# Optimization experiments

Hardware: AMD Instinct MI355X
Metric: run time of the kernel (lower is better)

## Reference

```python
import jax, jax.numpy as jnp
import numpy as np


def setup_inputs() -> dict:
    key = jax.random.key(0)
    k1, k2 = jax.random.split(key)
    image_features = jax.random.normal(k1, (8192, 128), dtype=jnp.float32)
    gts = jax.random.normal(k2, (16384, 128), dtype=jnp.float32)
    return {"image_features": image_features, "gts": gts}


def reference(image_features, gts):
    # (same math as subtract-square-sum-sqrt, O(N*M) memory instead of O(N*M*D))
    x_sq = jnp.sum(image_features * image_features, axis=-1, keepdims=True)  # [N,1]
    g_sq = jnp.sum(gts * gts, axis=-1)[None, :]                              # [1,M]
    xg = jnp.einsum('nd,md->nm', image_features, gts)                        # [N,M]
    d2 = jnp.maximum(x_sq + g_sq - 2.0 * xg, 0.0)
    logits = -jnp.sqrt(d2)
    return logits
```

## Files before the change

kernel.cpp:

```cpp
#include <hip/hip_runtime.h>


#define N_IMG 8192
#define N_GTS 16384
#define K_DIM 128
#define BM 128
#define BN 128
#define LDS_K 64
#define LDAH 72

typedef __attribute__((ext_vector_type(8))) short short8;
typedef __attribute__((ext_vector_type(4))) float f32x4;

__device__ __forceinline__ unsigned short f2bf(float x) {
    unsigned int u = __float_as_uint(x);
    u += 0x7FFFu + ((u >> 16) & 1u);
    return (unsigned short)(u >> 16);
}

__global__ __launch_bounds__(256, 2)
void l2sim_kernel(const float* __restrict__ A, const float* __restrict__ G,
                  float* __restrict__ out)
{
    __shared__ short a_s[BM][LDAH];
    __shared__ short b_s[BN][LDAH];
    __shared__ float xsq_s[2][BM];
    __shared__ float gsq_s[2][BN];

    const int t  = threadIdx.x;
    const int bm = blockIdx.y;
    const int bn = blockIdx.x;

    const int wave = t >> 6;
    const int lane = t & 63;
    const int wm   = (wave & 1) << 6;
    const int wn   = (wave >> 1) << 6;
    const int lm   = lane & 15;
    const int quad = lane >> 4;

    f32x4 acc[4][4] = {};

    #pragma unroll
    for (int h = 0; h < 2; ++h) {
        if (h) __syncthreads();

        {
            const float* gA = A + (size_t)bm * BM * K_DIM + h * LDS_K;
            #pragma unroll
            for (int i = 0; i < 8; ++i) {
                int f   = i * 256 + t;
                int row = f >> 4;
                int c4  = f & 15;
                float4 v = *(const float4*)(gA + (size_t)row * K_DIM + c4 * 4);
                float s = v.x*v.x + v.y*v.y + v.z*v.z + v.w*v.w;
                s += __shfl_down(s, 8, 16);
                s += __shfl_down(s, 4, 16);
                s += __shfl_down(s, 2, 16);
                s += __shfl_down(s, 1, 16);
                short4 bv;
                bv.x = (short)f2bf(v.x);
                bv.y = (short)f2bf(v.y);
                bv.z = (short)f2bf(v.z);
                bv.w = (short)f2bf(v.w);
                *(short4*)&a_s[row][c4 * 4] = bv;
                if ((t & 15) == 0) xsq_s[h][row] = s;
            }
        }
        {
            const float* gB = G + (size_t)bn * BN * K_DIM + h * LDS_K;
            #pragma unroll
            for (int i = 0; i < 8; ++i) {
                int f   = i * 256 + t;
                int row = f >> 4;
                int c4  = f & 15;
                float4 v = *(const float4*)(gB + (size_t)row * K_DIM + c4 * 4);
                float s = v.x*v.x + v.y*v.y + v.z*v.z + v.w*v.w;
                s += __shfl_down(s, 8, 16);
                s += __shfl_down(s, 4, 16);
                s += __shfl_down(s, 2, 16);
                s += __shfl_down(s, 1, 16);
                short4 bv;
                bv.x = (short)f2bf(v.x);
                bv.y = (short)f2bf(v.y);
                bv.z = (short)f2bf(v.z);
                bv.w = (short)f2bf(v.w);
                *(short4*)&b_s[row][c4 * 4] = bv;
                if ((t & 15) == 0) gsq_s[h][row] = s;
            }
        }
        __syncthreads();

        #pragma unroll
        for (int ks = 0; ks < 2; ++ks) {
            short8 af[4], bfr[4];
            #pragma unroll
            for (int mi = 0; mi < 4; ++mi)
                af[mi] = *(const short8*)&a_s[wm + mi * 16 + lm][ks * 32 + quad * 8];
            #pragma unroll
            for (int ni = 0; ni < 4; ++ni)
                bfr[ni] = *(const short8*)&b_s[wn + ni * 16 + lm][ks * 32 + quad * 8];
            #pragma unroll
            for (int mi = 0; mi < 4; ++mi)
                #pragma unroll
                for (int ni = 0; ni < 4; ++ni)
                    acc[mi][ni] = __builtin_amdgcn_mfma_f32_16x16x32_bf16(
                        af[mi], bfr[ni], acc[mi][ni], 0, 0, 0);
        }
    }

    float* outBase = out + (size_t)bm * BM * N_GTS + (size_t)bn * BN;
    #pragma unroll
    for (int mi = 0; mi < 4; ++mi) {
        #pragma unroll
        for (int r = 0; r < 4; ++r) {
            int m_loc = wm + mi * 16 + quad * 4 + r;
            float xs = xsq_s[0][m_loc] + xsq_s[1][m_loc];
            float* orow = outBase + (size_t)m_loc * N_GTS;
            #pragma unroll
            for (int ni = 0; ni < 4; ++ni) {
                int n_loc = wn + ni * 16 + lm;
                float gs = gsq_s[0][n_loc] + gsq_s[1][n_loc];
                float d2 = fmaxf(xs + gs - 2.0f * acc[mi][ni][r], 0.0f);
                orow[n_loc] = -sqrtf(d2);
            }
        }
    }
}

extern "C" void kernel_launch(void* const* d_in, const int* in_sizes, int n_in,
                              void* d_out, int out_size, void* d_ws, size_t ws_size,
                              hipStream_t stream) {
    const float* A = (const float*)d_in[0];
    const float* G = (const float*)d_in[1];
    float* out = (float*)d_out;
    dim3 grid(N_GTS / BN, N_IMG / BM);
    l2sim_kernel<<<grid, 256, 0, stream>>>(A, G, out);
}
```

Baseline: 796.9 us.

## Load MFMA fragments directly from global memory, dropping LDS staging and barriers

Each wave now reads its A and G fragments straight from global memory in MFMA layout, converts them with packed bf16 conversion instructions, and computes row norms in registers with cross-lane shuffles. This removes shared-memory staging, the block barriers and the software rounding routine. Occupancy hint rises to 3 blocks per CU. The cost is redundant global/L2 reads, since waves sharing a tile row or column reload the same data.

```diff
diff --git a/kernel.cpp b/kernel.cpp
--- a/kernel.cpp
+++ b/kernel.cpp
@@ -4,124 +4,90 @@
 #define N_IMG 8192
 #define N_GTS 16384
 #define K_DIM 128
-#define BM 128
-#define BN 128
-#define LDS_K 64
-#define LDAH 72
 
 typedef __attribute__((ext_vector_type(8))) short short8;
 typedef __attribute__((ext_vector_type(4))) float f32x4;
 
-__device__ __forceinline__ unsigned short f2bf(float x) {
-    unsigned int u = __float_as_uint(x);
-    u += 0x7FFFu + ((u >> 16) & 1u);
-    return (unsigned short)(u >> 16);
+__device__ __forceinline__ short8 cvt8(const float4& a, const float4& b) {
+    union { short8 s; unsigned int u[4]; } r;
+    asm("v_cvt_pk_bf16_f32 %0, %1, %2" : "=v"(r.u[0]) : "v"(a.x), "v"(a.y));
+    asm("v_cvt_pk_bf16_f32 %0, %1, %2" : "=v"(r.u[1]) : "v"(a.z), "v"(a.w));
+    asm("v_cvt_pk_bf16_f32 %0, %1, %2" : "=v"(r.u[2]) : "v"(b.x), "v"(b.y));
+    asm("v_cvt_pk_bf16_f32 %0, %1, %2" : "=v"(r.u[3]) : "v"(b.z), "v"(b.w));
+    return r.s;
 }
 
-__global__ __launch_bounds__(256, 2)
+__global__ __launch_bounds__(256, 3)
 void l2sim_kernel(const float* __restrict__ A, const float* __restrict__ G,
                   float* __restrict__ out)
 {
-    __shared__ short a_s[BM][LDAH];
-    __shared__ short b_s[BN][LDAH];
-    __shared__ float xsq_s[2][BM];
-    __shared__ float gsq_s[2][BN];
-
-    const int t  = threadIdx.x;
-    const int bm = blockIdx.y;
-    const int bn = blockIdx.x;
-
+    const int t    = threadIdx.x;
     const int wave = t >> 6;
     const int lane = t & 63;
-    const int wm   = (wave & 1) << 6;
-    const int wn   = (wave >> 1) << 6;
     const int lm   = lane & 15;
     const int quad = lane >> 4;
 
+    const int wtm = blockIdx.y * 128 + (wave & 1) * 64;
+    const int wtn = blockIdx.x * 128 + (wave >> 1) * 64;
+
+    const float* aRow[4];
+    const float* gRow[4];
+    #pragma unroll
+    for (int i = 0; i < 4; ++i) {
+        aRow[i] = A + (size_t)(wtm + i * 16 + lm) * K_DIM + quad * 8;
+        gRow[i] = G + (size_t)(wtn + i * 16 + lm) * K_DIM + quad * 8;
+    }
+
     f32x4 acc[4][4] = {};
+    float xsq[4] = {0.f, 0.f, 0.f, 0.f};
+    float gsq[4] = {0.f, 0.f, 0.f, 0.f};
 
     #pragma unroll
-    for (int h = 0; h < 2; ++h) {
-        if (h) __syncthreads();
-
-        {
-            const float* gA = A + (size_t)bm * BM * K_DIM + h * LDS_K;
-            #pragma unroll
-            for (int i = 0; i < 8; ++i) {
-                int f   = i * 256 + t;
-                int row = f >> 4;
-                int c4  = f & 15;
-                float4 v = *(const float4*)(gA + (size_t)row * K_DIM + c4 * 4);
-                float s = v.x*v.x + v.y*v.y + v.z*v.z + v.w*v.w;
-                s += __shfl_down(s, 8, 16);
-                s += __shfl_down(s, 4, 16);
-                s += __shfl_down(s, 2, 16);
-                s += __shfl_down(s, 1, 16);
-                short4 bv;
-                bv.x = (short)f2bf(v.x);
-                bv.y = (short)f2bf(v.y);
-                bv.z = (short)f2bf(v.z);
-                bv.w = (short)f2bf(v.w);
-                *(short4*)&a_s[row][c4 * 4] = bv;
-                if ((t & 15) == 0) xsq_s[h][row] = s;
-            }
+    for (int ks = 0; ks < 4; ++ks) {
+        short8 af[4], bfr[4];
+        #pragma unroll
+        for (int mi = 0; mi < 4; ++mi) {
+            float4 v0 = *(const float4*)(aRow[mi] + ks * 32);
+            float4 v1 = *(const float4*)(aRow[mi] + ks * 32 + 4);
+            xsq[mi] += v0.x*v0.x + v0.y*v0.y + v0.z*v0.z + v0.w*v0.w
+                     + v1.x*v1.x + v1.y*v1.y + v1.z*v1.z + v1.w*v1.w;
+            af[mi] = cvt8(v0, v1);
         }
-        {
-            const float* gB = G + (size_t)bn * BN * K_DIM + h * LDS_K;
-            #pragma unroll
-            for (int i = 0; i < 8; ++i) {
-                int f   = i * 256 + t;
-                int row = f >> 4;
-                int c4  = f & 15;
-                float4 v = *(const float4*)(gB + (size_t)row * K_DIM + c4 * 4);
-                float s = v.x*v.x + v.y*v.y + v.z*v.z + v.w*v.w;
-                s += __shfl_down(s, 8, 16);
-                s += __shfl_down(s, 4, 16);
-                s += __shfl_down(s, 2, 16);
-                s += __shfl_down(s, 1, 16);
-                short4 bv;
-                bv.x = (short)f2bf(v.x);
-                bv.y = (short)f2bf(v.y);
-                bv.z = (short)f2bf(v.z);
-                bv.w = (short)f2bf(v.w);
-                *(short4*)&b_s[row][c4 * 4] = bv;
-                if ((t & 15) == 0) gsq_s[h][row] = s;
-            }
+        #pragma unroll
+        for (int ni = 0; ni < 4; ++ni) {
+            float4 v0 = *(const float4*)(gRow[ni] + ks * 32);
+            float4 v1 = *(const float4*)(gRow[ni] + ks * 32 + 4);
+            gsq[ni] += v0.x*v0.x + v0.y*v0.y + v0.z*v0.z + v0.w*v0.w
+                     + v1.x*v1.x + v1.y*v1.y + v1.z*v1.z + v1.w*v1.w;
+            bfr[ni] = cvt8(v0, v1);
         }
-        __syncthreads();
-
         #pragma unroll
-        for (int ks = 0; ks < 2; ++ks) {
-            short8 af[4], bfr[4];
-            #pragma unroll
-            for (int mi = 0; mi < 4; ++mi)
-                af[mi] = *(const short8*)&a_s[wm + mi * 16 + lm][ks * 32 + quad * 8];
+        for (int mi = 0; mi < 4; ++mi)
             #pragma unroll
             for (int ni = 0; ni < 4; ++ni)
-                bfr[ni] = *(const short8*)&b_s[wn + ni * 16 + lm][ks * 32 + quad * 8];
-            #pragma unroll
-            for (int mi = 0; mi < 4; ++mi)
-                #pragma unroll
-                for (int ni = 0; ni < 4; ++ni)
-                    acc[mi][ni] = __builtin_amdgcn_mfma_f32_16x16x32_bf16(
-                        af[mi], bfr[ni], acc[mi][ni], 0, 0, 0);
-        }
+                acc[mi][ni] = __builtin_amdgcn_mfma_f32_16x16x32_bf16(
+                    af[mi], bfr[ni], acc[mi][ni], 0, 0, 0);
     }
 
-    float* outBase = out + (size_t)bm * BM * N_GTS + (size_t)bn * BN;
+    #pragma unroll
+    for (int i = 0; i < 4; ++i) {
+        xsq[i] += __shfl_xor(xsq[i], 16);
+        xsq[i] += __shfl_xor(xsq[i], 32);
+        gsq[i] += __shfl_xor(gsq[i], 16);
+        gsq[i] += __shfl_xor(gsq[i], 32);
+    }
+
+    float* outBase = out + (size_t)wtm * N_GTS + wtn;
     #pragma unroll
     for (int mi = 0; mi < 4; ++mi) {
         #pragma unroll
         for (int r = 0; r < 4; ++r) {
-            int m_loc = wm + mi * 16 + quad * 4 + r;
-            float xs = xsq_s[0][m_loc] + xsq_s[1][m_loc];
-            float* orow = outBase + (size_t)m_loc * N_GTS;
+            float xs = __shfl(xsq[mi], quad * 4 + r);
+            float* orow = outBase + (size_t)(mi * 16 + quad * 4 + r) * N_GTS;
             #pragma unroll
             for (int ni = 0; ni < 4; ++ni) {
-                int n_loc = wn + ni * 16 + lm;
-                float gs = gsq_s[0][n_loc] + gsq_s[1][n_loc];
-                float d2 = fmaxf(xs + gs - 2.0f * acc[mi][ni][r], 0.0f);
-                orow[n_loc] = -sqrtf(d2);
+                float d2 = fmaxf(xs + gsq[ni] - 2.0f * acc[mi][ni][r], 0.0f);
+                orow[ni * 16 + lm] = -sqrtf(d2);
             }
         }
     }
@@ -133,6 +99,6 @@
     const float* A = (const float*)d_in[0];
     const float* G = (const float*)d_in[1];
     float* out = (float*)d_out;
-    dim3 grid(N_GTS / BN, N_IMG / BM);
+    dim3 grid(N_GTS / 128, N_IMG / 128);
     l2sim_kernel<<<grid, 256, 0, stream>>>(A, G, out);
 }
```

After: 746.7 us. 6.3% less time.
